# Kernel tuning notes

Measured on AMD Instinct MI355X. Metric: run time of the kernel, lower is better.

## Reference

```python
import jax, jax.numpy as jnp
from jax import lax
import numpy as np

K_UP = 5
SCALE = 2


def _cbs(x, w, s, b, groups=1):
    # yolov5 Conv: conv2d(bias=False, pad=k//2) + BN(eval, folded into scale/bias) + SiLU
    y = lax.conv_general_dilated(x, w, (1, 1), 'SAME',
                                 dimension_numbers=('NCHW', 'OIHW', 'NCHW'),
                                 feature_group_count=groups)
    y = y * s[None, :, None, None] + b[None, :, None, None]
    return y * jax.nn.sigmoid(y)


def _msgconv(x, p):
    (cv1_w, cv1_s, cv1_b, dw3_w, dw3_s, dw3_b,
     dw5_w, dw5_s, dw5_b, px_w, px_s, px_b) = p
    x1 = _cbs(x, cv1_w, cv1_s, cv1_b)                      # [b, min_ch, h, w]
    ch = x1.shape[1] // 2
    # rearrange 'bs (g ch) h w -> bs ch h w g' with g=2: group0=ch[:half], group1=ch[half:]
    g0 = _cbs(x1[:, :ch], dw3_w, dw3_s, dw3_b, groups=ch)  # depthwise k=3
    g1 = _cbs(x1[:, ch:], dw5_w, dw5_s, dw5_b, groups=ch)  # depthwise k=5
    x2 = jnp.concatenate([g0, g1], axis=1)
    return _cbs(jnp.concatenate([x1, x2], axis=1), px_w, px_s, px_b)


def _carafe(X, comp_p, enc_p):
    b, c, h, w = X.shape
    r, k = SCALE, K_UP
    k2 = k * k
    W = _msgconv(_msgconv(X, comp_p), enc_p)               # [b, (r*k)^2, h, w]
    # PixelShuffle(r): [b, k2*r^2, h, w] -> [b, k2, h*r, w*r]
    W = W.reshape(b, k2, r, r, h, w).transpose(0, 1, 4, 2, 5, 3).reshape(b, k2, h * r, w * r)
    W = jax.nn.softmax(W, axis=1)
    # nearest upsample by r
    Xu = jnp.repeat(jnp.repeat(X, r, axis=2), r, axis=3)   # [b, c, h_, w_]
    h_, w_ = h * r, w * r
    pad = (k // 2) * r                                      # 4
    Xp = jnp.pad(Xu, ((0, 0), (0, 0), (pad, pad), (pad, pad)))
    # Unfold(kernel=k, dilation=r, padding=pad): kernel pos (p,q) -> offset r*p, r*q in padded map
    patches = jnp.stack([Xp[:, :, r * p:r * p + h_, r * q:r * q + w_]
                         for p in range(k) for q in range(k)], axis=2)  # [b, c, k2, h_, w_]
    return jnp.einsum('bkhw,bckhw->bchw', W, patches)


def _conv_params(key, cout, cin, k):
    k1, k2, k3 = jax.random.split(key, 3)
    w = jax.random.normal(k1, (cout, cin, k, k), jnp.float32) / np.float32(np.sqrt(cin * k * k))
    s = 1.0 + 0.1 * jax.random.normal(k2, (cout,), jnp.float32)
    b = 0.1 * jax.random.normal(k3, (cout,), jnp.float32)
    return w, s, b


def setup_inputs() -> dict:
    key = jax.random.key(0)
    ks = jax.random.split(key, 9)
    c, c_mid = 128, 64
    enc_out = (SCALE * K_UP) ** 2  # 100
    d = {'X': jax.random.normal(ks[0], (2, c, 64, 64), jnp.float32)}
    mc = c_mid // 2                # 32
    d['comp_cv1_w'], d['comp_cv1_s'], d['comp_cv1_b'] = _conv_params(ks[1], mc, c, 1)
    d['comp_dw3_w'], d['comp_dw3_s'], d['comp_dw3_b'] = _conv_params(ks[2], mc // 2, 1, 3)
    d['comp_dw5_w'], d['comp_dw5_s'], d['comp_dw5_b'] = _conv_params(ks[3], mc // 2, 1, 5)
    d['comp_px_w'], d['comp_px_s'], d['comp_px_b'] = _conv_params(ks[4], c_mid, c_mid, 1)
    me = enc_out // 2              # 50
    d['enc_cv1_w'], d['enc_cv1_s'], d['enc_cv1_b'] = _conv_params(ks[5], me, c_mid, 1)
    d['enc_dw3_w'], d['enc_dw3_s'], d['enc_dw3_b'] = _conv_params(ks[6], me // 2, 1, 3)
    d['enc_dw5_w'], d['enc_dw5_s'], d['enc_dw5_b'] = _conv_params(ks[7], me // 2, 1, 5)
    d['enc_px_w'], d['enc_px_s'], d['enc_px_b'] = _conv_params(ks[8], enc_out, enc_out, 1)
    return d


def reference(X, comp_cv1_w, comp_cv1_s, comp_cv1_b, comp_dw3_w, comp_dw3_s, comp_dw3_b,
              comp_dw5_w, comp_dw5_s, comp_dw5_b, comp_px_w, comp_px_s, comp_px_b,
              enc_cv1_w, enc_cv1_s, enc_cv1_b, enc_dw3_w, enc_dw3_s, enc_dw3_b,
              enc_dw5_w, enc_dw5_s, enc_dw5_b, enc_px_w, enc_px_s, enc_px_b):
    comp_p = (comp_cv1_w, comp_cv1_s, comp_cv1_b, comp_dw3_w, comp_dw3_s, comp_dw3_b,
              comp_dw5_w, comp_dw5_s, comp_dw5_b, comp_px_w, comp_px_s, comp_px_b)
    enc_p = (enc_cv1_w, enc_cv1_s, enc_cv1_b, enc_dw3_w, enc_dw3_s, enc_dw3_b,
             enc_dw5_w, enc_dw5_s, enc_dw5_b, enc_px_w, enc_px_s, enc_px_b)
    return _carafe(X, comp_p, enc_p)
```

## Files before the change

### kernel.cpp

```cpp
#include <hip/hip_runtime.h>
#include <math.h>

__device__ __forceinline__ float silu_act(float y) {
    return y / (1.f + __expf(-y));
}

template<int TC, int CIN>
__global__ void pw_conv_silu(const float* __restrict__ in, int HW, int B,
                             const float* __restrict__ w,
                             const float* __restrict__ sc, const float* __restrict__ bi,
                             float* __restrict__ out, int CoutStride) {
    int g = blockIdx.x * blockDim.x + threadIdx.x;
    if (g >= B * HW) return;
    int b = g / HW, pix = g - b * HW;
    int co0 = blockIdx.y * TC;
    float acc[TC];
#pragma unroll
    for (int j = 0; j < TC; ++j) acc[j] = 0.f;
    const float* ip = in + (size_t)b * CIN * HW + pix;
    const float* wp = w + (size_t)co0 * CIN;
#pragma unroll 8
    for (int ci = 0; ci < CIN; ++ci) {
        float v = ip[(size_t)ci * HW];
#pragma unroll
        for (int j = 0; j < TC; ++j)
            acc[j] = fmaf(v, wp[j * CIN + ci], acc[j]);
    }
#pragma unroll
    for (int j = 0; j < TC; ++j) {
        int co = co0 + j;
        float y = fmaf(acc[j], sc[co], bi[co]);
        out[((size_t)b * CoutStride + co) * HW + pix] = silu_act(y);
    }
}

__global__ void dw_conv_silu(float* __restrict__ cat, int ch, int H, int W, int Ctot, int B,
                             const float* __restrict__ w3, const float* __restrict__ s3,
                             const float* __restrict__ b3,
                             const float* __restrict__ w5, const float* __restrict__ s5,
                             const float* __restrict__ b5) {
    int HW = H * W;
    int idx = blockIdx.x * blockDim.x + threadIdx.x;
    int total = B * 2 * ch * HW;
    if (idx >= total) return;
    int pix = idx % HW;
    int t = idx / HW;
    int c2 = t % (2 * ch);
    int b = t / (2 * ch);
    int x = pix % W, y = pix / W;
    const float* ip = cat + ((size_t)b * Ctot + c2) * HW;
    float acc = 0.f, scale, bias;
    if (c2 < ch) {
        const float* wk = w3 + c2 * 9;
#pragma unroll
        for (int ky = 0; ky < 3; ++ky) {
            int iy = y + ky - 1;
            if ((unsigned)iy >= (unsigned)H) continue;
#pragma unroll
            for (int kx = 0; kx < 3; ++kx) {
                int ix = x + kx - 1;
                if ((unsigned)ix >= (unsigned)W) continue;
                acc = fmaf(ip[iy * W + ix], wk[ky * 3 + kx], acc);
            }
        }
        scale = s3[c2]; bias = b3[c2];
    } else {
        int c = c2 - ch;
        const float* wk = w5 + c * 25;
#pragma unroll
        for (int ky = 0; ky < 5; ++ky) {
            int iy = y + ky - 2;
            if ((unsigned)iy >= (unsigned)H) continue;
#pragma unroll
            for (int kx = 0; kx < 5; ++kx) {
                int ix = x + kx - 2;
                if ((unsigned)ix >= (unsigned)W) continue;
                acc = fmaf(ip[iy * W + ix], wk[ky * 5 + kx], acc);
            }
        }
        scale = s5[c]; bias = b5[c];
    }
    float v = fmaf(acc, scale, bias);
    cat[((size_t)b * Ctot + 2 * ch + c2) * HW + pix] = silu_act(v);
}

__global__ void carafe_kernel(const float* __restrict__ X, const float* __restrict__ Wenc,
                              float* __restrict__ out) {
    const int H = 64, Wd = 64, C = 128, Ho = 128, Wo = 128, HW = H * Wd;
    int Y = blockIdx.x;
    int cchunk = blockIdx.y;
    int b = blockIdx.z;
    __shared__ float xs[32][5][64];
    __shared__ float sw[2][25][2][64];
    int t = threadIdx.x;

    const float* wb = Wenc + (size_t)b * 100 * HW + (size_t)Y * Wd;
    for (int i = t; i < 2 * 25 * 128; i += 256) {
        int l = i & 63;
        int par = (i >> 6) & 1;
        int j = (i >> 7) % 25;
        int r = i / (128 * 25);
        int chW = j * 4 + r * 2 + par;
        sw[r][j][par][l] = wb[(size_t)chW * HW + l];
    }
    int c0 = cchunk * 32;
    const float* Xb = X + ((size_t)b * C + c0) * HW;
    for (int i = t; i < 32 * 5 * 64; i += 256) {
        int x = i & 63;
        int p = (i >> 6) % 5;
        int c = i / (64 * 5);
        int iy = Y + p - 2;
        xs[c][p][x] = ((unsigned)iy < (unsigned)H) ? Xb[(size_t)c * HW + iy * Wd + x] : 0.f;
    }
    __syncthreads();

    {
        int l = t & 63;
        int par = (t >> 6) & 1;
        int r = t >> 7;
        float m = -1e30f;
#pragma unroll
        for (int j = 0; j < 25; ++j) m = fmaxf(m, sw[r][j][par][l]);
        float e[25];
        float s = 0.f;
#pragma unroll
        for (int j = 0; j < 25; ++j) { e[j] = __expf(sw[r][j][par][l] - m); s += e[j]; }
        float inv = 1.f / s;
#pragma unroll
        for (int j = 0; j < 25; ++j) sw[r][j][par][l] = e[j] * inv;
    }
    __syncthreads();

    int l = t & 63;
    int tc = t >> 6;
    for (int k = 0; k < 8; ++k) {
        int c = tc * 8 + k;
        float xv[25];
#pragma unroll
        for (int p = 0; p < 5; ++p)
#pragma unroll
            for (int q = 0; q < 5; ++q) {
                int ix = l + q - 2;
                xv[p * 5 + q] = ((unsigned)ix < (unsigned)Wd) ? xs[c][p][ix] : 0.f;
            }
        float a00 = 0.f, a01 = 0.f, a10 = 0.f, a11 = 0.f;
#pragma unroll
        for (int j = 0; j < 25; ++j) {
            float v = xv[j];
            a00 = fmaf(sw[0][j][0][l], v, a00);
            a01 = fmaf(sw[0][j][1][l], v, a01);
            a10 = fmaf(sw[1][j][0][l], v, a10);
            a11 = fmaf(sw[1][j][1][l], v, a11);
        }
        size_t ob = (((size_t)b * C + (c0 + c)) * Ho + 2 * Y) * Wo;
        *reinterpret_cast<float2*>(&out[ob + 2 * l])      = make_float2(a00, a01);
        *reinterpret_cast<float2*>(&out[ob + Wo + 2 * l]) = make_float2(a10, a11);
    }
}

extern "C" void kernel_launch(void* const* d_in, const int* in_sizes, int n_in,
                              void* d_out, int out_size, void* d_ws, size_t ws_size,
                              hipStream_t stream) {
    const float* X          = (const float*)d_in[0];
    const float* comp_cv1_w = (const float*)d_in[1];
    const float* comp_cv1_s = (const float*)d_in[2];
    const float* comp_cv1_b = (const float*)d_in[3];
    const float* comp_dw3_w = (const float*)d_in[4];
    const float* comp_dw3_s = (const float*)d_in[5];
    const float* comp_dw3_b = (const float*)d_in[6];
    const float* comp_dw5_w = (const float*)d_in[7];
    const float* comp_dw5_s = (const float*)d_in[8];
    const float* comp_dw5_b = (const float*)d_in[9];
    const float* comp_px_w  = (const float*)d_in[10];
    const float* comp_px_s  = (const float*)d_in[11];
    const float* comp_px_b  = (const float*)d_in[12];
    const float* enc_cv1_w  = (const float*)d_in[13];
    const float* enc_cv1_s  = (const float*)d_in[14];
    const float* enc_cv1_b  = (const float*)d_in[15];
    const float* enc_dw3_w  = (const float*)d_in[16];
    const float* enc_dw3_s  = (const float*)d_in[17];
    const float* enc_dw3_b  = (const float*)d_in[18];
    const float* enc_dw5_w  = (const float*)d_in[19];
    const float* enc_dw5_s  = (const float*)d_in[20];
    const float* enc_dw5_b  = (const float*)d_in[21];
    const float* enc_px_w   = (const float*)d_in[22];
    const float* enc_px_s   = (const float*)d_in[23];
    const float* enc_px_b   = (const float*)d_in[24];
    float* out = (float*)d_out;

    const int B = 2, H = 64, W = 64, HW = H * W;
    float* cat_c  = (float*)d_ws;
    float* y_comp = cat_c  + (size_t)B * 64 * HW;
    float* cat_e  = y_comp + (size_t)B * 64 * HW;
    float* wraw   = cat_e  + (size_t)B * 100 * HW;

    int pixBlocks = (B * HW + 255) / 256;

    pw_conv_silu<4, 128><<<dim3(pixBlocks, 8), 256, 0, stream>>>(
        X, HW, B, comp_cv1_w, comp_cv1_s, comp_cv1_b, cat_c, 64);
    {
        int n = B * 32 * HW;
        dw_conv_silu<<<(n + 255) / 256, 256, 0, stream>>>(
            cat_c, 16, H, W, 64, B,
            comp_dw3_w, comp_dw3_s, comp_dw3_b,
            comp_dw5_w, comp_dw5_s, comp_dw5_b);
    }
    pw_conv_silu<4, 64><<<dim3(pixBlocks, 16), 256, 0, stream>>>(
        cat_c, HW, B, comp_px_w, comp_px_s, comp_px_b, y_comp, 64);

    pw_conv_silu<5, 64><<<dim3(pixBlocks, 10), 256, 0, stream>>>(
        y_comp, HW, B, enc_cv1_w, enc_cv1_s, enc_cv1_b, cat_e, 100);
    {
        int n = B * 50 * HW;
        dw_conv_silu<<<(n + 255) / 256, 256, 0, stream>>>(
            cat_e, 25, H, W, 100, B,
            enc_dw3_w, enc_dw3_s, enc_dw3_b,
            enc_dw5_w, enc_dw5_s, enc_dw5_b);
    }
    pw_conv_silu<5, 100><<<dim3(pixBlocks, 20), 256, 0, stream>>>(
        cat_e, HW, B, enc_px_w, enc_px_s, enc_px_b, wraw, 100);

    carafe_kernel<<<dim3(64, 4, B), 256, 0, stream>>>(X, wraw, out);
}
```

Before: 90.30 us.

## Fuse encoder pointwise conv with softmax and keep CARAFE weights in registers

Replaces the final encoder pointwise conv with a per-row kernel that stages the row in LDS, computes all 25 kernel logits per subpixel phase in registers, applies SiLU and softmax, and writes normalized weights in a [b][Y][phase][j][x] layout. The CARAFE kernel no longer does softmax. It loads its 100 weights per thread straight into registers, uses a zero-padded X tile to drop bounds checks, and halves the channel chunk to 16 so there are twice as many blocks. This removes the separate softmax pass and its LDS traffic. In exchange it uses heavy per-thread registers (100 inputs plus 25 accumulators in wprep, 100 weights in carafe), and wprep launches only 128 blocks, so parallelism is low.

```diff
diff --git a/kernel.cpp b/kernel.cpp
--- a/kernel.cpp
+++ b/kernel.cpp
@@ -84,77 +84,104 @@
     cat[((size_t)b * Ctot + 2 * ch + c2) * HW + pix] = silu_act(v);
 }
 
-__global__ void carafe_kernel(const float* __restrict__ X, const float* __restrict__ Wenc,
-                              float* __restrict__ out) {
+__global__ __launch_bounds__(256) void wprep_kernel(
+        const float* __restrict__ cat_e, const float* __restrict__ w,
+        const float* __restrict__ sc, const float* __restrict__ bi,
+        float* __restrict__ ws) {
+    const int HW = 4096;
+    int Y = blockIdx.x;
+    int b = blockIdx.y;
+    __shared__ float le[100][64];
+    int t = threadIdx.x;
+    const float* src = cat_e + (size_t)b * 100 * HW + Y * 64;
+    for (int i = t; i < 100 * 64; i += 256) {
+        int ci = i >> 6, x = i & 63;
+        le[ci][x] = src[(size_t)ci * HW + x];
+    }
+    __syncthreads();
+    int l = t & 63;
+    int g = __builtin_amdgcn_readfirstlane(t >> 6);
+    float xr[100];
+#pragma unroll
+    for (int ci = 0; ci < 100; ++ci) xr[ci] = le[ci][l];
+    float acc[25];
+#pragma unroll
+    for (int j = 0; j < 25; ++j) acc[j] = 0.f;
+#pragma unroll 4
+    for (int ci = 0; ci < 100; ++ci) {
+        float xv = xr[ci];
+#pragma unroll
+        for (int j = 0; j < 25; ++j)
+            acc[j] = fmaf(xv, w[(j * 4 + g) * 100 + ci], acc[j]);
+    }
+    float m = -1e30f;
+#pragma unroll
+    for (int j = 0; j < 25; ++j) {
+        int co = j * 4 + g;
+        acc[j] = silu_act(fmaf(acc[j], sc[co], bi[co]));
+        m = fmaxf(m, acc[j]);
+    }
+    float s = 0.f;
+#pragma unroll
+    for (int j = 0; j < 25; ++j) { acc[j] = __expf(acc[j] - m); s += acc[j]; }
+    float inv = 1.f / s;
+    float* dst = ws + ((((size_t)b * 64 + Y) * 4 + g) * 25) * 64 + l;
+#pragma unroll
+    for (int j = 0; j < 25; ++j) dst[j * 64] = acc[j] * inv;
+}
+
+__global__ __launch_bounds__(256) void carafe_kernel(
+        const float* __restrict__ X, const float* __restrict__ ws,
+        float* __restrict__ out) {
     const int H = 64, Wd = 64, C = 128, Ho = 128, Wo = 128, HW = H * Wd;
     int Y = blockIdx.x;
     int cchunk = blockIdx.y;
     int b = blockIdx.z;
-    __shared__ float xs[32][5][64];
-    __shared__ float sw[2][25][2][64];
+    __shared__ float xs[16][5][68];
     int t = threadIdx.x;
-
-    const float* wb = Wenc + (size_t)b * 100 * HW + (size_t)Y * Wd;
-    for (int i = t; i < 2 * 25 * 128; i += 256) {
-        int l = i & 63;
-        int par = (i >> 6) & 1;
-        int j = (i >> 7) % 25;
-        int r = i / (128 * 25);
-        int chW = j * 4 + r * 2 + par;
-        sw[r][j][par][l] = wb[(size_t)chW * HW + l];
-    }
-    int c0 = cchunk * 32;
+    int c0 = cchunk * 16;
     const float* Xb = X + ((size_t)b * C + c0) * HW;
-    for (int i = t; i < 32 * 5 * 64; i += 256) {
-        int x = i & 63;
-        int p = (i >> 6) % 5;
-        int c = i / (64 * 5);
+    for (int i = t; i < 16 * 5 * 68; i += 256) {
+        int col = i % 68;
+        int tmp = i / 68;
+        int p = tmp % 5;
+        int c = tmp / 5;
         int iy = Y + p - 2;
-        xs[c][p][x] = ((unsigned)iy < (unsigned)H) ? Xb[(size_t)c * HW + iy * Wd + x] : 0.f;
-    }
-    __syncthreads();
-
-    {
-        int l = t & 63;
-        int par = (t >> 6) & 1;
-        int r = t >> 7;
-        float m = -1e30f;
-#pragma unroll
-        for (int j = 0; j < 25; ++j) m = fmaxf(m, sw[r][j][par][l]);
-        float e[25];
-        float s = 0.f;
-#pragma unroll
-        for (int j = 0; j < 25; ++j) { e[j] = __expf(sw[r][j][par][l] - m); s += e[j]; }
-        float inv = 1.f / s;
-#pragma unroll
-        for (int j = 0; j < 25; ++j) sw[r][j][par][l] = e[j] * inv;
-    }
-    __syncthreads();
-
+        int ix = col - 2;
+        float v = 0.f;
+        if ((unsigned)iy < (unsigned)H && (unsigned)ix < (unsigned)Wd)
+            v = Xb[(size_t)c * HW + iy * Wd + ix];
+        xs[c][p][col] = v;
+    }
     int l = t & 63;
     int tc = t >> 6;
-    for (int k = 0; k < 8; ++k) {
-        int c = tc * 8 + k;
-        float xv[25];
+    const float* wsrow = ws + (((size_t)b * 64 + Y) * 100) * 64 + l;
+    float wreg[4][25];
+#pragma unroll
+    for (int rp = 0; rp < 4; ++rp)
+#pragma unroll
+        for (int j = 0; j < 25; ++j)
+            wreg[rp][j] = wsrow[(rp * 25 + j) * 64];
+    __syncthreads();
+
+#pragma unroll
+    for (int k = 0; k < 4; ++k) {
+        int c = tc * 4 + k;
+        float a00 = 0.f, a01 = 0.f, a10 = 0.f, a11 = 0.f;
 #pragma unroll
         for (int p = 0; p < 5; ++p)
 #pragma unroll
             for (int q = 0; q < 5; ++q) {
-                int ix = l + q - 2;
-                xv[p * 5 + q] = ((unsigned)ix < (unsigned)Wd) ? xs[c][p][ix] : 0.f;
+                float v = xs[c][p][l + q];
+                int j = p * 5 + q;
+                a00 = fmaf(wreg[0][j], v, a00);
+                a01 = fmaf(wreg[1][j], v, a01);
+                a10 = fmaf(wreg[2][j], v, a10);
+                a11 = fmaf(wreg[3][j], v, a11);
             }
-        float a00 = 0.f, a01 = 0.f, a10 = 0.f, a11 = 0.f;
-#pragma unroll
-        for (int j = 0; j < 25; ++j) {
-            float v = xv[j];
-            a00 = fmaf(sw[0][j][0][l], v, a00);
-            a01 = fmaf(sw[0][j][1][l], v, a01);
-            a10 = fmaf(sw[1][j][0][l], v, a10);
-            a11 = fmaf(sw[1][j][1][l], v, a11);
-        }
-        size_t ob = (((size_t)b * C + (c0 + c)) * Ho + 2 * Y) * Wo;
-        *reinterpret_cast<float2*>(&out[ob + 2 * l])      = make_float2(a00, a01);
-        *reinterpret_cast<float2*>(&out[ob + Wo + 2 * l]) = make_float2(a10, a11);
+        size_t ob = (((size_t)b * C + (c0 + c)) * Ho + 2 * Y) * Wo + 2 * l;
+        *reinterpret_cast<float2*>(&out[ob])      = make_float2(a00, a01);
+        *reinterpret_cast<float2*>(&out[ob + Wo]) = make_float2(a10, a11);
     }
 }
 
@@ -192,7 +219,7 @@
     float* cat_c  = (float*)d_ws;
     float* y_comp = cat_c  + (size_t)B * 64 * HW;
     float* cat_e  = y_comp + (size_t)B * 64 * HW;
-    float* wraw   = cat_e  + (size_t)B * 100 * HW;
+    float* ws     = cat_e  + (size_t)B * 100 * HW;
 
     int pixBlocks = (B * HW + 255) / 256;
 
@@ -217,8 +244,9 @@
             enc_dw3_w, enc_dw3_s, enc_dw3_b,
             enc_dw5_w, enc_dw5_s, enc_dw5_b);
     }
-    pw_conv_silu<5, 100><<<dim3(pixBlocks, 20), 256, 0, stream>>>(
-        cat_e, HW, B, enc_px_w, enc_px_s, enc_px_b, wraw, 100);
-
-    carafe_kernel<<<dim3(64, 4, B), 256, 0, stream>>>(X, wraw, out);
-}
+
+    wprep_kernel<<<dim3(64, B), 256, 0, stream>>>(
+        cat_e, enc_px_w, enc_px_s, enc_px_b, ws);
+
+    carafe_kernel<<<dim3(64, 8, B), 256, 0, stream>>>(X, ws, out);
+}
```

After: 96.10 us. +6.4%, slower.
